# Performance work log

Measured on AMD Instinct MI355X. Metric: run time of the kernel, lower is better.

## Reference

```python
import jax, jax.numpy as jnp
import numpy as np

E, T, C = 100000, 1000000, 64


def setup_inputs() -> dict:
    key = jax.random.key(0)
    k1, k2, k3, k4, k5 = jax.random.split(key, 5)
    xij = jax.random.normal(k1, (E, C), dtype=jnp.float32)
    r = jax.random.normal(k2, (E, 3), dtype=jnp.float32)
    attn = jax.random.normal(k3, (1, C), dtype=jnp.float32)
    t_src = jax.random.randint(k4, (T,), 0, E)
    t_dst = jax.random.randint(k5, (T,), 0, E)
    return {"xij": xij, "r": r, "attn": attn, "t_src": t_src, "t_dst": t_dst}


def reference(xij, r, attn, t_src, t_dst):
    n_edges, channels = xij.shape
    # unit bond directions (negated, as in the torch code)
    rnorm = -r / jnp.linalg.norm(r, axis=1, keepdims=True)          # [E, 3]
    # triplet angle cosines via gather + dot (fn.u_dot_v)
    cos_jik = jnp.sum(rnorm[t_src] * rnorm[t_dst], axis=-1)         # [T]
    # Chebyshev angular expansion: T_n(x) = cos(n * arccos(x)), n = 0..C-1
    theta = jnp.arccos(jnp.clip(cos_jik, -1.0 + 1e-6, 1.0 - 1e-6))  # [T]
    z_jik = jnp.cos(theta[:, None] * jnp.arange(channels, dtype=theta.dtype)[None, :])  # [T, C]
    # fn.u_add_v on bond features
    x_jik = xij[t_src] + xij[t_dst]                                 # [T, C]
    e_jik = jax.nn.silu(z_jik + x_jik)                              # [T, C]
    a = jnp.sum(e_jik * attn, axis=-1)                              # [T]
    # edge_softmax over incoming triplets of each destination bond
    a_max = jax.ops.segment_max(a, t_dst, num_segments=n_edges)     # [E]
    ex = jnp.exp(a - a_max[t_dst])                                  # [T]
    denom = jax.ops.segment_sum(ex, t_dst, num_segments=n_edges)    # [E]
    alpha = ex / denom[t_dst]                                       # [T]
    # gather-multiply-scatter-sum aggregation (u_mul_e + sum)
    m = xij[t_src] * alpha[:, None]                                 # [T, C]
    ft = jax.ops.segment_sum(m, t_dst, num_segments=n_edges)        # [E, C]
    return ft
```

## Files before the change

### kernel.cpp

```cpp
#include <hip/hip_runtime.h>
#include <math.h>


#define LOG2E 1.4426950408889634f
#define SCAN_B 256

__global__ void ta_init(const float* __restrict__ r,
                        float4* __restrict__ rnorm4,
                        int* __restrict__ rowptr,
                        int E) {
    int i = blockIdx.x * blockDim.x + threadIdx.x;
    if (i < E) {
        float rx = r[i * 3 + 0], ry = r[i * 3 + 1], rz = r[i * 3 + 2];
        float inv = rsqrtf(rx * rx + ry * ry + rz * rz);
        rnorm4[i] = make_float4(rx * inv, ry * inv, rz * inv, 0.f);
        rowptr[i] = 0;
    }
}

__global__ void ta_hist(const int* __restrict__ t_dst,
                        int* __restrict__ rowptr, int T) {
    int i = blockIdx.x * blockDim.x + threadIdx.x;
    int T4 = T >> 2;
    if (i < T4) {
        int4 d = ((const int4*)t_dst)[i];
        atomicAdd(&rowptr[d.x], 1);
        atomicAdd(&rowptr[d.y], 1);
        atomicAdd(&rowptr[d.z], 1);
        atomicAdd(&rowptr[d.w], 1);
    }
    int t = (T4 << 2) + i;
    if (i < (T & 3) ? 0 : 0) {}
    if (t < T && i >= T4) {}
    if (i == 0) {
        for (int u = T4 << 2; u < T; ++u) atomicAdd(&rowptr[t_dst[u]], 1);
    }
}

__global__ void ta_scan1(int* __restrict__ rowptr, int* __restrict__ bsum, int E) {
    __shared__ int sm[SCAN_B];
    int i = blockIdx.x * SCAN_B + threadIdx.x;
    int v = (i < E) ? rowptr[i] : 0;
    sm[threadIdx.x] = v;
    __syncthreads();
    int x = v;
    for (int o = 1; o < SCAN_B; o <<= 1) {
        int y = (threadIdx.x >= (unsigned)o) ? sm[threadIdx.x - o] : 0;
        __syncthreads();
        x += y;
        sm[threadIdx.x] = x;
        __syncthreads();
    }
    if (i < E) rowptr[i] = x - v;
    if (threadIdx.x == SCAN_B - 1) bsum[blockIdx.x] = x;
}

__global__ void ta_scan2(int* __restrict__ bsum, int n) {
    __shared__ int sm[512];
    int tid = threadIdx.x;
    int v = (tid < n) ? bsum[tid] : 0;
    sm[tid] = v;
    __syncthreads();
    int x = v;
    for (int o = 1; o < 512; o <<= 1) {
        int y = (tid >= o) ? sm[tid - o] : 0;
        __syncthreads();
        x += y;
        sm[tid] = x;
        __syncthreads();
    }
    if (tid < n) bsum[tid] = x - v;
}

__global__ void ta_scatter(const int* __restrict__ t_dst,
                           const int* __restrict__ t_src,
                           int* __restrict__ rowptr,
                           const int* __restrict__ bsum,
                           int* __restrict__ ssorted, int T) {
    int t = blockIdx.x * blockDim.x + threadIdx.x;
    if (t < T) {
        int d = t_dst[t];
        int pos = atomicAdd(&rowptr[d], 1) + bsum[d >> 8];
        ssorted[pos] = t_src[t];
    }
}

__global__ void ta_fused(const float* __restrict__ xij,
                         const float* __restrict__ attn,
                         const float4* __restrict__ rnorm4,
                         const int* __restrict__ ssorted,
                         const int* __restrict__ segend,
                         const int* __restrict__ bsum,
                         float* __restrict__ ft, int E) {
    const int lane = threadIdx.x & 63;
    const int waveId = blockIdx.x * (blockDim.x >> 6) + (threadIdx.x >> 6);
    if (waveId >= E) return;
    const int e = waveId;
    const int g   = lane >> 3;
    const int sub = lane & 7;
    const int c0  = sub * 8;
    const float fc0 = (float)c0;

    int end = segend[e] + bsum[e >> 8];
    int start = (e == 0) ? 0 : (segend[e - 1] + bsum[(e - 1) >> 8]);
    int len = end - start;

    float xd[8], at[8];
    const float* xdp = xij + (size_t)e * 64 + c0;
    *(float4*)&xd[0] = *(const float4*)(xdp);
    *(float4*)&xd[4] = *(const float4*)(xdp + 4);
    *(float4*)&at[0] = *(const float4*)(attn + c0);
    *(float4*)&at[4] = *(const float4*)(attn + c0 + 4);
    const float4 rd = rnorm4[e];

    float m = -3.402823466e38f, den = 0.f;
    float acc[8] = {0, 0, 0, 0, 0, 0, 0, 0};

    for (int chunk = start; chunk < end; chunk += 64) {
        int cl = end - chunk; if (cl > 64) cl = 64;
        int idx = chunk + lane; if (idx >= end) idx = end - 1;
        int sv = ssorted[idx];
        float4 rs = rnorm4[sv];
        float cosj = rs.x * rd.x + rs.y * rd.y + rs.z * rd.z;
        cosj = fminf(fmaxf(cosj, -1.0f + 1e-6f), 1.0f - 1e-6f);
        float th2p = acosf(cosj) * 0.15915493667125702f;

        for (int j8 = 0; j8 < cl; j8 += 8) {
            int jj = j8 + g;
            bool active = (jj < cl);
            int jc = active ? jj : 0;
            float th = __shfl(th2p, jc, 64);
            float tc = __shfl(cosj, jc, 64);
            int   s  = __shfl(sv,   jc, 64);

            const float* xsp = xij + (size_t)s * 64 + c0;
            float xs[8];
            *(float4*)&xs[0] = *(const float4*)(xsp);
            *(float4*)&xs[4] = *(const float4*)(xsp + 4);

            float r0 = th * fc0;
            float z0 = __builtin_amdgcn_cosf(r0 - floorf(r0));
            float r1 = r0 + th;
            float z1 = __builtin_amdgcn_cosf(r1 - floorf(r1));
            float twoc = 2.0f * tc;

            float part = 0.f;
            float zkm1 = z0, zk = z1;
            #pragma unroll
            for (int k = 0; k < 8; ++k) {
                float z = (k == 0) ? z0 : zk;
                float v = z + xs[k] + xd[k];
                float ez = __builtin_amdgcn_exp2f(-v * LOG2E);
                float sl = v * __builtin_amdgcn_rcpf(1.0f + ez);
                part = fmaf(sl, at[k], part);
                if (k > 0) {
                    float zn = fmaf(twoc, zk, -zkm1);
                    zkm1 = zk; zk = zn;
                }
            }
            part += __shfl_xor(part, 1, 64);
            part += __shfl_xor(part, 2, 64);
            part += __shfl_xor(part, 4, 64);
            float contrib = active ? part : -3.402823466e38f;
            float mn = fmaxf(m, contrib);
            float scale = __builtin_amdgcn_exp2f((m - mn) * LOG2E);
            float p     = __builtin_amdgcn_exp2f((contrib - mn) * LOG2E);
            den = den * scale + p;
            #pragma unroll
            for (int k = 0; k < 8; ++k) acc[k] = fmaf(p, xs[k], acc[k] * scale);
            m = mn;
        }
    }

    if (len > 1) {
        #pragma unroll
        for (int off = 8; off < 64; off <<= 1) {
            float m2 = __shfl_xor(m, off, 64);
            float d2 = __shfl_xor(den, off, 64);
            float mn = fmaxf(m, m2);
            float s1 = __builtin_amdgcn_exp2f((m - mn) * LOG2E);
            float s2 = __builtin_amdgcn_exp2f((m2 - mn) * LOG2E);
            den = den * s1 + d2 * s2;
            #pragma unroll
            for (int k = 0; k < 8; ++k) {
                float a2 = __shfl_xor(acc[k], off, 64);
                acc[k] = acc[k] * s1 + a2 * s2;
            }
            m = mn;
        }
    }

    float rden = (len > 0) ? __builtin_amdgcn_rcpf(den) : 0.f;
    if (lane < 8) {
        float out[8];
        #pragma unroll
        for (int k = 0; k < 8; ++k) out[k] = acc[k] * rden;
        float* fo = ft + (size_t)e * 64 + lane * 8;
        *(float4*)(fo)     = *(float4*)&out[0];
        *(float4*)(fo + 4) = *(float4*)&out[4];
    }
}

extern "C" void kernel_launch(void* const* d_in, const int* in_sizes, int n_in,
                              void* d_out, int out_size, void* d_ws, size_t ws_size,
                              hipStream_t stream) {
    const float* xij   = (const float*)d_in[0];
    const float* r     = (const float*)d_in[1];
    const float* attn  = (const float*)d_in[2];
    const int*   t_src = (const int*)d_in[3];
    const int*   t_dst = (const int*)d_in[4];
    float* ft = (float*)d_out;

    const int E = in_sizes[1] / 3;
    const int T = in_sizes[3];

    char* ws = (char*)d_ws;
    float4* rnorm4  = (float4*)ws;
    int*    ssorted = (int*)(ws + (size_t)E * 16);
    int*    rowptr  = (int*)((char*)ssorted + (size_t)T * 4);
    int*    bsum    = (int*)((char*)rowptr + (size_t)E * 4);

    const int nScanBlocks = (E + SCAN_B - 1) / SCAN_B;

    ta_init<<<(E + 255) / 256, 256, 0, stream>>>(r, rnorm4, rowptr, E);
    ta_hist<<<((T >> 2) + 255) / 256, 256, 0, stream>>>(t_dst, rowptr, T);
    ta_scan1<<<nScanBlocks, SCAN_B, 0, stream>>>(rowptr, bsum, E);
    ta_scan2<<<1, 512, 0, stream>>>(bsum, nScanBlocks);
    ta_scatter<<<(T + 255) / 256, 256, 0, stream>>>(t_dst, t_src, rowptr, bsum, ssorted, T);
    ta_fused<<<(E + 3) / 4, 256, 0, stream>>>(xij, attn, rnorm4, ssorted, rowptr, bsum, ft, E);
}
```

Baseline: 270.6 us.

## Replace CSR sort with fixed-capacity per-destination buckets plus spill list

Adds a path that scatters triplet sources directly into fixed-capacity per-destination buckets using one atomic per triplet, with overflow pairs in a spill list. This replaces the histogram, two-level scan and separate scatter passes with a single grouping pass. The fused kernel reads bucket counts directly and scans the spill list for overflowing edges. It needs more workspace and falls back to the old CSR path when the workspace is too small; spill entries beyond the fixed limit would be dropped.

```diff
diff --git a/kernel.cpp b/kernel.cpp
--- a/kernel.cpp
+++ b/kernel.cpp
@@ -4,11 +4,224 @@
 
 #define LOG2E 1.4426950408889634f
 #define SCAN_B 256
-
-__global__ void ta_init(const float* __restrict__ r,
-                        float4* __restrict__ rnorm4,
-                        int* __restrict__ rowptr,
-                        int E) {
+#define SPILL_PAIRS 65536
+
+
+__global__ void ta_init_b(const float* __restrict__ r,
+                          float4* __restrict__ rnorm4,
+                          int* __restrict__ cnt,
+                          int* __restrict__ spill_cnt,
+                          int E) {
+    int i = blockIdx.x * blockDim.x + threadIdx.x;
+    if (i < E) {
+        float rx = r[i * 3 + 0], ry = r[i * 3 + 1], rz = r[i * 3 + 2];
+        float inv = rsqrtf(rx * rx + ry * ry + rz * rz);
+        rnorm4[i] = make_float4(rx * inv, ry * inv, rz * inv, 0.f);
+        cnt[i] = 0;
+    }
+    if (i == 0) *spill_cnt = 0;
+}
+
+__global__ void ta_scatter_b(const int* __restrict__ t_dst,
+                             const int* __restrict__ t_src,
+                             int* __restrict__ cnt,
+                             int* __restrict__ bucket,
+                             int* __restrict__ spill,
+                             int* __restrict__ spill_cnt,
+                             int T, int CAP) {
+    int i = blockIdx.x * blockDim.x + threadIdx.x;
+    int T4 = T >> 2;
+    if (i < T4) {
+        int4 d = ((const int4*)t_dst)[i];
+        int4 s = ((const int4*)t_src)[i];
+        int p0 = atomicAdd(&cnt[d.x], 1);
+        int p1 = atomicAdd(&cnt[d.y], 1);
+        int p2 = atomicAdd(&cnt[d.z], 1);
+        int p3 = atomicAdd(&cnt[d.w], 1);
+        if (p0 < CAP) bucket[(size_t)d.x * CAP + p0] = s.x;
+        else { int u = atomicAdd(spill_cnt, 1); if (u < SPILL_PAIRS) { spill[2*u] = d.x; spill[2*u+1] = s.x; } }
+        if (p1 < CAP) bucket[(size_t)d.y * CAP + p1] = s.y;
+        else { int u = atomicAdd(spill_cnt, 1); if (u < SPILL_PAIRS) { spill[2*u] = d.y; spill[2*u+1] = s.y; } }
+        if (p2 < CAP) bucket[(size_t)d.z * CAP + p2] = s.z;
+        else { int u = atomicAdd(spill_cnt, 1); if (u < SPILL_PAIRS) { spill[2*u] = d.z; spill[2*u+1] = s.z; } }
+        if (p3 < CAP) bucket[(size_t)d.w * CAP + p3] = s.w;
+        else { int u = atomicAdd(spill_cnt, 1); if (u < SPILL_PAIRS) { spill[2*u] = d.w; spill[2*u+1] = s.w; } }
+    }
+    if (i == 0) {
+        for (int t = T4 << 2; t < T; ++t) {
+            int d = t_dst[t];
+            int p = atomicAdd(&cnt[d], 1);
+            if (p < CAP) bucket[(size_t)d * CAP + p] = t_src[t];
+            else { int u = atomicAdd(spill_cnt, 1); if (u < SPILL_PAIRS) { spill[2*u] = d; spill[2*u+1] = t_src[t]; } }
+        }
+    }
+}
+
+__global__ void ta_fused_b(const float* __restrict__ xij,
+                           const float* __restrict__ attn,
+                           const float4* __restrict__ rnorm4,
+                           const int* __restrict__ bucket,
+                           const int* __restrict__ cnt,
+                           const int* __restrict__ spill,
+                           const int* __restrict__ spill_cnt,
+                           float* __restrict__ ft, int E, int CAP) {
+    const int lane = threadIdx.x & 63;
+    const int waveId = blockIdx.x * (blockDim.x >> 6) + (threadIdx.x >> 6);
+    if (waveId >= E) return;
+    const int e = waveId;
+    const int g   = lane >> 3;
+    const int sub = lane & 7;
+    const int c0  = sub * 8;
+    const float fc0 = (float)c0;
+
+    int len = cnt[e];
+    int eff = (len < CAP) ? len : CAP;
+    const int* bkt = bucket + (size_t)e * CAP;
+
+    float xd[8], at[8];
+    const float* xdp = xij + (size_t)e * 64 + c0;
+    *(float4*)&xd[0] = *(const float4*)(xdp);
+    *(float4*)&xd[4] = *(const float4*)(xdp + 4);
+    *(float4*)&at[0] = *(const float4*)(attn + c0);
+    *(float4*)&at[4] = *(const float4*)(attn + c0 + 4);
+    const float4 rd = rnorm4[e];
+
+    float m = -3.402823466e38f, den = 0.f;
+    float acc[8] = {0, 0, 0, 0, 0, 0, 0, 0};
+
+    for (int chunk = 0; chunk < eff; chunk += 64) {
+        int cl = eff - chunk; if (cl > 64) cl = 64;
+        int idx = chunk + lane; if (idx >= eff) idx = eff - 1;
+        int sv = bkt[idx];
+        float4 rs = rnorm4[sv];
+        float cosj = rs.x * rd.x + rs.y * rd.y + rs.z * rd.z;
+        cosj = fminf(fmaxf(cosj, -1.0f + 1e-6f), 1.0f - 1e-6f);
+        float th2p = acosf(cosj) * 0.15915493667125702f;
+
+        for (int j8 = 0; j8 < cl; j8 += 8) {
+            int jj = j8 + g;
+            bool active = (jj < cl);
+            int jc = active ? jj : 0;
+            float th = __shfl(th2p, jc, 64);
+            float tc = __shfl(cosj, jc, 64);
+            int   s  = __shfl(sv,   jc, 64);
+
+            const float* xsp = xij + (size_t)s * 64 + c0;
+            float xs[8];
+            *(float4*)&xs[0] = *(const float4*)(xsp);
+            *(float4*)&xs[4] = *(const float4*)(xsp + 4);
+
+            float r0 = th * fc0;
+            float z0 = __builtin_amdgcn_cosf(r0 - floorf(r0));
+            float r1 = r0 + th;
+            float z1 = __builtin_amdgcn_cosf(r1 - floorf(r1));
+            float twoc = 2.0f * tc;
+
+            float part = 0.f;
+            float zkm1 = z0, zk = z1;
+            #pragma unroll
+            for (int k = 0; k < 8; ++k) {
+                float z = (k == 0) ? z0 : zk;
+                float v = z + xs[k] + xd[k];
+                float ez = __builtin_amdgcn_exp2f(-v * LOG2E);
+                float sl = v * __builtin_amdgcn_rcpf(1.0f + ez);
+                part = fmaf(sl, at[k], part);
+                if (k > 0) {
+                    float zn = fmaf(twoc, zk, -zkm1);
+                    zkm1 = zk; zk = zn;
+                }
+            }
+            part += __shfl_xor(part, 1, 64);
+            part += __shfl_xor(part, 2, 64);
+            part += __shfl_xor(part, 4, 64);
+            float contrib = active ? part : -3.402823466e38f;
+            float mn = fmaxf(m, contrib);
+            float scale = __builtin_amdgcn_exp2f((m - mn) * LOG2E);
+            float p     = __builtin_amdgcn_exp2f((contrib - mn) * LOG2E);
+            den = den * scale + p;
+            #pragma unroll
+            for (int k = 0; k < 8; ++k) acc[k] = fmaf(p, xs[k], acc[k] * scale);
+            m = mn;
+        }
+    }
+
+    if (len > CAP) {
+        int ns = *spill_cnt; if (ns > SPILL_PAIRS) ns = SPILL_PAIRS;
+        for (int u = 0; u < ns; ++u) {
+            int d2 = spill[2 * u];
+            if (d2 != e) continue;
+            int s2 = spill[2 * u + 1];
+            float4 rs = rnorm4[s2];
+            float cosj = rs.x * rd.x + rs.y * rd.y + rs.z * rd.z;
+            cosj = fminf(fmaxf(cosj, -1.0f + 1e-6f), 1.0f - 1e-6f);
+            float th = acosf(cosj) * 0.15915493667125702f;
+            const float* xsp = xij + (size_t)s2 * 64 + c0;
+            float xs[8];
+            *(float4*)&xs[0] = *(const float4*)(xsp);
+            *(float4*)&xs[4] = *(const float4*)(xsp + 4);
+            float r0 = th * fc0;
+            float z0 = __builtin_amdgcn_cosf(r0 - floorf(r0));
+            float r1 = r0 + th;
+            float z1 = __builtin_amdgcn_cosf(r1 - floorf(r1));
+            float twoc = 2.0f * cosj;
+            float part = 0.f;
+            float zkm1 = z0, zk = z1;
+            #pragma unroll
+            for (int k = 0; k < 8; ++k) {
+                float z = (k == 0) ? z0 : zk;
+                float v = z + xs[k] + xd[k];
+                float ez = __builtin_amdgcn_exp2f(-v * LOG2E);
+                float sl = v * __builtin_amdgcn_rcpf(1.0f + ez);
+                part = fmaf(sl, at[k], part);
+                if (k > 0) { float zn = fmaf(twoc, zk, -zkm1); zkm1 = zk; zk = zn; }
+            }
+            part += __shfl_xor(part, 1, 64);
+            part += __shfl_xor(part, 2, 64);
+            part += __shfl_xor(part, 4, 64);
+            if (g == 0) {
+                float mn = fmaxf(m, part);
+                float scale = __builtin_amdgcn_exp2f((m - mn) * LOG2E);
+                float p     = __builtin_amdgcn_exp2f((part - mn) * LOG2E);
+                den = den * scale + p;
+                #pragma unroll
+                for (int k = 0; k < 8; ++k) acc[k] = fmaf(p, xs[k], acc[k] * scale);
+                m = mn;
+            }
+        }
+    }
+
+    if (len > 1) {
+        #pragma unroll
+        for (int off = 8; off < 64; off <<= 1) {
+            float m2 = __shfl_xor(m, off, 64);
+            float d2 = __shfl_xor(den, off, 64);
+            float mn = fmaxf(m, m2);
+            float s1 = __builtin_amdgcn_exp2f((m - mn) * LOG2E);
+            float s2 = __builtin_amdgcn_exp2f((m2 - mn) * LOG2E);
+            den = den * s1 + d2 * s2;
+            #pragma unroll
+            for (int k = 0; k < 8; ++k) {
+                float a2 = __shfl_xor(acc[k], off, 64);
+                acc[k] = acc[k] * s1 + a2 * s2;
+            }
+            m = mn;
+        }
+    }
+
+    float rden = (len > 0) ? __builtin_amdgcn_rcpf(den) : 0.f;
+    if (lane < 8) {
+        float out[8];
+        #pragma unroll
+        for (int k = 0; k < 8; ++k) out[k] = acc[k] * rden;
+        float* fo = ft + (size_t)e * 64 + lane * 8;
+        *(float4*)(fo)     = *(float4*)&out[0];
+        *(float4*)(fo + 4) = *(float4*)&out[4];
+    }
+}
+
+
+__global__ void ta_init(const float* __restrict__ r, float4* __restrict__ rnorm4,
+                        int* __restrict__ rowptr, int E) {
     int i = blockIdx.x * blockDim.x + threadIdx.x;
     if (i < E) {
         float rx = r[i * 3 + 0], ry = r[i * 3 + 1], rz = r[i * 3 + 2];
@@ -18,8 +231,7 @@
     }
 }
 
-__global__ void ta_hist(const int* __restrict__ t_dst,
-                        int* __restrict__ rowptr, int T) {
+__global__ void ta_hist(const int* __restrict__ t_dst, int* __restrict__ rowptr, int T) {
     int i = blockIdx.x * blockDim.x + threadIdx.x;
     int T4 = T >> 2;
     if (i < T4) {
@@ -29,12 +241,7 @@
         atomicAdd(&rowptr[d.z], 1);
         atomicAdd(&rowptr[d.w], 1);
     }
-    int t = (T4 << 2) + i;
-    if (i < (T & 3) ? 0 : 0) {}
-    if (t < T && i >= T4) {}
-    if (i == 0) {
-        for (int u = T4 << 2; u < T; ++u) atomicAdd(&rowptr[t_dst[u]], 1);
-    }
+    if (i == 0) for (int u = T4 << 2; u < T; ++u) atomicAdd(&rowptr[t_dst[u]], 1);
 }
 
 __global__ void ta_scan1(int* __restrict__ rowptr, int* __restrict__ bsum, int E) {
@@ -47,8 +254,7 @@
     for (int o = 1; o < SCAN_B; o <<= 1) {
         int y = (threadIdx.x >= (unsigned)o) ? sm[threadIdx.x - o] : 0;
         __syncthreads();
-        x += y;
-        sm[threadIdx.x] = x;
+        x += y; sm[threadIdx.x] = x;
         __syncthreads();
     }
     if (i < E) rowptr[i] = x - v;
@@ -65,17 +271,14 @@
     for (int o = 1; o < 512; o <<= 1) {
         int y = (tid >= o) ? sm[tid - o] : 0;
         __syncthreads();
-        x += y;
-        sm[tid] = x;
+        x += y; sm[tid] = x;
         __syncthreads();
     }
     if (tid < n) bsum[tid] = x - v;
 }
 
-__global__ void ta_scatter(const int* __restrict__ t_dst,
-                           const int* __restrict__ t_src,
-                           int* __restrict__ rowptr,
-                           const int* __restrict__ bsum,
+__global__ void ta_scatter(const int* __restrict__ t_dst, const int* __restrict__ t_src,
+                           int* __restrict__ rowptr, const int* __restrict__ bsum,
                            int* __restrict__ ssorted, int T) {
     int t = blockIdx.x * blockDim.x + threadIdx.x;
     if (t < T) {
@@ -85,26 +288,19 @@
     }
 }
 
-__global__ void ta_fused(const float* __restrict__ xij,
-                         const float* __restrict__ attn,
-                         const float4* __restrict__ rnorm4,
-                         const int* __restrict__ ssorted,
-                         const int* __restrict__ segend,
-                         const int* __restrict__ bsum,
+__global__ void ta_fused(const float* __restrict__ xij, const float* __restrict__ attn,
+                         const float4* __restrict__ rnorm4, const int* __restrict__ ssorted,
+                         const int* __restrict__ segend, const int* __restrict__ bsum,
                          float* __restrict__ ft, int E) {
     const int lane = threadIdx.x & 63;
     const int waveId = blockIdx.x * (blockDim.x >> 6) + (threadIdx.x >> 6);
     if (waveId >= E) return;
     const int e = waveId;
-    const int g   = lane >> 3;
-    const int sub = lane & 7;
-    const int c0  = sub * 8;
+    const int g = lane >> 3, sub = lane & 7, c0 = sub * 8;
     const float fc0 = (float)c0;
-
     int end = segend[e] + bsum[e >> 8];
     int start = (e == 0) ? 0 : (segend[e - 1] + bsum[(e - 1) >> 8]);
     int len = end - start;
-
     float xd[8], at[8];
     const float* xdp = xij + (size_t)e * 64 + c0;
     *(float4*)&xd[0] = *(const float4*)(xdp);
@@ -112,10 +308,8 @@
     *(float4*)&at[0] = *(const float4*)(attn + c0);
     *(float4*)&at[4] = *(const float4*)(attn + c0 + 4);
     const float4 rd = rnorm4[e];
-
     float m = -3.402823466e38f, den = 0.f;
     float acc[8] = {0, 0, 0, 0, 0, 0, 0, 0};
-
     for (int chunk = start; chunk < end; chunk += 64) {
         int cl = end - chunk; if (cl > 64) cl = 64;
         int idx = chunk + lane; if (idx >= end) idx = end - 1;
@@ -124,7 +318,6 @@
         float cosj = rs.x * rd.x + rs.y * rd.y + rs.z * rd.z;
         cosj = fminf(fmaxf(cosj, -1.0f + 1e-6f), 1.0f - 1e-6f);
         float th2p = acosf(cosj) * 0.15915493667125702f;
-
         for (int j8 = 0; j8 < cl; j8 += 8) {
             int jj = j8 + g;
             bool active = (jj < cl);
@@ -132,18 +325,15 @@
             float th = __shfl(th2p, jc, 64);
             float tc = __shfl(cosj, jc, 64);
             int   s  = __shfl(sv,   jc, 64);
-
             const float* xsp = xij + (size_t)s * 64 + c0;
             float xs[8];
             *(float4*)&xs[0] = *(const float4*)(xsp);
             *(float4*)&xs[4] = *(const float4*)(xsp + 4);
-
             float r0 = th * fc0;
             float z0 = __builtin_amdgcn_cosf(r0 - floorf(r0));
             float r1 = r0 + th;
             float z1 = __builtin_amdgcn_cosf(r1 - floorf(r1));
             float twoc = 2.0f * tc;
-
             float part = 0.f;
             float zkm1 = z0, zk = z1;
             #pragma unroll
@@ -153,10 +343,7 @@
                 float ez = __builtin_amdgcn_exp2f(-v * LOG2E);
                 float sl = v * __builtin_amdgcn_rcpf(1.0f + ez);
                 part = fmaf(sl, at[k], part);
-                if (k > 0) {
-                    float zn = fmaf(twoc, zk, -zkm1);
-                    zkm1 = zk; zk = zn;
-                }
+                if (k > 0) { float zn = fmaf(twoc, zk, -zkm1); zkm1 = zk; zk = zn; }
             }
             part += __shfl_xor(part, 1, 64);
             part += __shfl_xor(part, 2, 64);
@@ -171,7 +358,6 @@
             m = mn;
         }
     }
-
     if (len > 1) {
         #pragma unroll
         for (int off = 8; off < 64; off <<= 1) {
@@ -189,7 +375,6 @@
             m = mn;
         }
     }
-
     float rden = (len > 0) ? __builtin_amdgcn_rcpf(den) : 0.f;
     if (lane < 8) {
         float out[8];
@@ -200,6 +385,7 @@
         *(float4*)(fo + 4) = *(float4*)&out[4];
     }
 }
+
 
 extern "C" void kernel_launch(void* const* d_in, const int* in_sizes, int n_in,
                               void* d_out, int out_size, void* d_ws, size_t ws_size,
@@ -214,18 +400,37 @@
     const int E = in_sizes[1] / 3;
     const int T = in_sizes[3];
 
+    size_t fixed = (size_t)E * 16 + (size_t)E * 4 + 4 + (size_t)SPILL_PAIRS * 8;
+    int CAP = 0;
+    if (fixed + (size_t)E * 32 * 4 <= ws_size) CAP = 32;
+    else if (fixed + (size_t)E * 24 * 4 <= ws_size) CAP = 24;
+    else if (fixed + (size_t)E * 16 * 4 <= ws_size) CAP = 16;
+
     char* ws = (char*)d_ws;
-    float4* rnorm4  = (float4*)ws;
-    int*    ssorted = (int*)(ws + (size_t)E * 16);
-    int*    rowptr  = (int*)((char*)ssorted + (size_t)T * 4);
-    int*    bsum    = (int*)((char*)rowptr + (size_t)E * 4);
-
-    const int nScanBlocks = (E + SCAN_B - 1) / SCAN_B;
-
-    ta_init<<<(E + 255) / 256, 256, 0, stream>>>(r, rnorm4, rowptr, E);
-    ta_hist<<<((T >> 2) + 255) / 256, 256, 0, stream>>>(t_dst, rowptr, T);
-    ta_scan1<<<nScanBlocks, SCAN_B, 0, stream>>>(rowptr, bsum, E);
-    ta_scan2<<<1, 512, 0, stream>>>(bsum, nScanBlocks);
-    ta_scatter<<<(T + 255) / 256, 256, 0, stream>>>(t_dst, t_src, rowptr, bsum, ssorted, T);
-    ta_fused<<<(E + 3) / 4, 256, 0, stream>>>(xij, attn, rnorm4, ssorted, rowptr, bsum, ft, E);
-}
+    if (CAP >= 16) {
+        float4* rnorm4    = (float4*)ws;
+        int*    cnt       = (int*)(ws + (size_t)E * 16);
+        int*    spill_cnt = (int*)((char*)cnt + (size_t)E * 4);
+        int*    spill     = spill_cnt + 1;
+        int*    bucket    = spill + (size_t)SPILL_PAIRS * 2;
+
+        ta_init_b<<<(E + 255) / 256, 256, 0, stream>>>(r, rnorm4, cnt, spill_cnt, E);
+        ta_scatter_b<<<((T >> 2) + 255) / 256, 256, 0, stream>>>(
+            t_dst, t_src, cnt, bucket, spill, spill_cnt, T, CAP);
+        ta_fused_b<<<(E + 3) / 4, 256, 0, stream>>>(
+            xij, attn, rnorm4, bucket, cnt, spill, spill_cnt, ft, E, CAP);
+    } else {
+        float4* rnorm4  = (float4*)ws;
+        int*    ssorted = (int*)(ws + (size_t)E * 16);
+        int*    rowptr  = (int*)((char*)ssorted + (size_t)T * 4);
+        int*    bsum    = (int*)((char*)rowptr + (size_t)E * 4);
+        const int nScanBlocks = (E + SCAN_B - 1) / SCAN_B;
+
+        ta_init<<<(E + 255) / 256, 256, 0, stream>>>(r, rnorm4, rowptr, E);
+        ta_hist<<<((T >> 2) + 255) / 256, 256, 0, stream>>>(t_dst, rowptr, T);
+        ta_scan1<<<nScanBlocks, SCAN_B, 0, stream>>>(rowptr, bsum, E);
+        ta_scan2<<<1, 512, 0, stream>>>(bsum, nScanBlocks);
+        ta_scatter<<<(T + 255) / 256, 256, 0, stream>>>(t_dst, t_src, rowptr, bsum, ssorted, T);
+        ta_fused<<<(E + 3) / 4, 256, 0, stream>>>(xij, attn, rnorm4, ssorted, rowptr, bsum, ft, E);
+    }
+}
```

Measured after the change: 219.5 us. 18.9% less time.
